# Optimization experiments

Hardware: AMD Instinct MI355X
Metric: run time of the kernel (lower is better)

Reference implementation:

```python
import jax, jax.numpy as jnp
import numpy as np


def setup_inputs() -> dict:
    key = jax.random.key(0)
    B, T, I, H = 64, 512, 1024, 1024
    ks = jax.random.split(key, 9)
    scale_x = 1.0 / np.sqrt(I)
    scale_h = 1.0 / np.sqrt(H)
    inp = {"x": jax.random.normal(ks[0], (B, T, I), jnp.float32)}
    names = [("wxi", "whi"), ("wxf", "whf"), ("wxg", "whg"), ("wxo", "who")]
    for g, (nx, nh) in enumerate(names):
        inp[nx] = jax.random.normal(ks[1 + 2 * g], (I, H), jnp.float32) * scale_x
        inp[nh] = jax.random.normal(ks[2 + 2 * g], (H, H), jnp.float32) * scale_h
    for b in ["bxi", "bhi", "bxf", "bhf", "bxg", "bhg", "bxo", "bho"]:
        inp[b] = jnp.zeros((H,), jnp.float32)
    return inp


def reference(x, wxi, bxi, whi, bhi, wxf, bxf, whf, bhf,
              wxg, bxg, whg, bhg, wxo, bxo, who, bho):
    B, T, I = x.shape
    H = whi.shape[0]
    # Precompute all input projections in one big GEMM: (B,T,4H)
    wx = jnp.concatenate([wxi, wxf, wxg, wxo], axis=1)            # (I,4H)
    bx = jnp.concatenate([bxi + bhi, bxf + bhf, bxg + bhg, bxo + bho])  # fold both biases
    xproj = jnp.einsum('bti,ih->bth', x, wx) + bx                 # (B,T,4H)
    wh = jnp.concatenate([whi, whf, whg, who], axis=1)            # (H,4H)

    def step(carry, xp_t):
        h, c = carry                                              # (B,H) each
        gates = xp_t + h @ wh                                     # (B,4H)
        i, f, g, o = jnp.split(gates, 4, axis=-1)
        i = jax.nn.sigmoid(i)
        f = jax.nn.sigmoid(f)
        g = jnp.tanh(g)
        o = jax.nn.sigmoid(o)
        c = f * c + i * g
        h = o * jnp.tanh(c)
        return (h, c), None

    h0 = jnp.zeros((B, H), x.dtype)
    c0 = jnp.zeros((B, H), x.dtype)
    (h_t, c_t), _ = jax.lax.scan(step, (h0, c0), jnp.swapaxes(xproj, 0, 1))
    return (h_t, c_t)
```

## Files before the change

### kernel.cpp

```cpp
#include <hip/hip_runtime.h>

typedef short bf16x8 __attribute__((ext_vector_type(8)));
typedef float f32x4 __attribute__((ext_vector_type(4)));
typedef unsigned long long u64x2 __attribute__((ext_vector_type(2)));

__device__ __forceinline__ unsigned short f2bf(float f) {
  unsigned u = __float_as_uint(f);
  unsigned r = (u + 0x7FFFu + ((u >> 16) & 1u)) >> 16;
  return (unsigned short)r;
}
__device__ __forceinline__ float bf2f(unsigned short s) {
  return __uint_as_float(((unsigned)s) << 16);
}
__device__ __forceinline__ float sigm(float x) {
  return __builtin_amdgcn_rcpf(1.f + __expf(-x));
}
__device__ __forceinline__ float tanh_a(float x) {
  return 1.f - 2.f * __builtin_amdgcn_rcpf(__expf(2.f * x) + 1.f);
}

__device__ __forceinline__ void gload_lds16(const void* g, void* l) {
  __builtin_amdgcn_global_load_lds(
      (const __attribute__((address_space(1))) unsigned int*)g,
      (__attribute__((address_space(3))) unsigned int*)l, 16, 0, 0);
}

#define ALOAD(p)     __hip_atomic_load((p), __ATOMIC_RELAXED, __HIP_MEMORY_SCOPE_AGENT)
#define ASTORE(p, v) __hip_atomic_store((p), (v), __ATOMIC_RELAXED, __HIP_MEMORY_SCOPE_AGENT)


__global__ void k_cvt_x(const float* __restrict__ x, unsigned short* __restrict__ xb, int n4) {
  int i = blockIdx.x * blockDim.x + threadIdx.x;
  if (i < n4) {
    float4 v = ((const float4*)x)[i];
    ushort4 o;
    o.x = f2bf(v.x); o.y = f2bf(v.y); o.z = f2bf(v.z); o.w = f2bf(v.w);
    ((ushort4*)xb)[i] = o;
  }
}

__global__ void k_pack_w(const float* __restrict__ wxi, const float* __restrict__ wxf,
                         const float* __restrict__ wxg, const float* __restrict__ wxo,
                         const float* __restrict__ whi, const float* __restrict__ whf,
                         const float* __restrict__ whg, const float* __restrict__ who,
                         unsigned short* __restrict__ wxt, unsigned short* __restrict__ whp) {
  const float* srcs[8] = {wxi, wxf, wxg, wxo, whi, whf, whg, who};
  int slab = blockIdx.z;
  const float* src = srcs[slab];
  int gate = slab & 3;
  bool is_wh = slab >= 4;
  __shared__ float tile[32][33];
  int tx = threadIdx.x, ty = threadIdx.y;
  int j0 = blockIdx.x * 32, k0 = blockIdx.y * 32;
  #pragma unroll
  for (int i = 0; i < 32; i += 8)
    tile[ty + i][tx] = src[(size_t)(k0 + ty + i) * 1024 + j0 + tx];
  __syncthreads();
  unsigned short* dst = is_wh ? whp : wxt;
  #pragma unroll
  for (int i = 0; i < 32; i += 8) {
    int j = j0 + ty + i;
    int k = k0 + tx;
    float v = tile[tx][ty + i];
    int row = is_wh ? ((j >> 2) * 16 + gate * 4 + (j & 3)) : (gate * 1024 + j);
    dst[(size_t)row * 1024 + k] = f2bf(v);
  }
}

__global__ void k_bias(const float* bxi, const float* bhi, const float* bxf, const float* bhf,
                       const float* bxg, const float* bhg, const float* bxo, const float* bho,
                       float* __restrict__ bx4) {
  int n = blockIdx.x * 256 + threadIdx.x;
  int gate = n >> 10, j = n & 1023;
  const float* a = gate == 0 ? bxi : gate == 1 ? bxf : gate == 2 ? bxg : bxo;
  const float* b = gate == 0 ? bhi : gate == 1 ? bhf : gate == 2 ? bhg : bho;
  bx4[n] = a[j] + b[j];
}

__global__ void k_init(unsigned short* __restrict__ hbuf, unsigned int* __restrict__ flags) {
  int i = blockIdx.x * 256 + threadIdx.x;
  ASTORE((unsigned long long*)hbuf + i, 0ull);
  if (i < 256) ASTORE(flags + i, 0u);
}


__global__ __launch_bounds__(256) void k_xproj(
    const unsigned short* __restrict__ xb,
    const unsigned short* __restrict__ wxt,
    const float* __restrict__ bx4,
    unsigned short* __restrict__ xp)
{
  __shared__ __align__(16) short As[128 * 64];
  __shared__ __align__(16) short Bs[128 * 64];
  const int tid = threadIdx.x;
  const int bid = blockIdx.x;
  const int m0 = (bid >> 5) * 128;
  const int n0 = (bid & 31) * 128;
  const int lane = tid & 63, w = tid >> 6;
  const int l15 = lane & 15, hi = lane >> 4;
  const int mrow0 = (w >> 1) * 64, ncol0 = (w & 1) * 64;

  f32x4 acc[4][4] = {};
  const char* xbB = (const char*)xb;
  const char* wtB = (const char*)wxt;

  for (int ks = 0; ks < 16; ++ks) {
    #pragma unroll
    for (int c = 0; c < 4; ++c) {
      int d = c * 4096 + tid * 16;
      int r = d >> 7;
      int kb = (d & 127) ^ ((r & 7) << 4);
      gload_lds16(xbB + ((size_t)(m0 + r) * 2048 + ks * 128 + kb), (char*)As + d);
    }
    #pragma unroll
    for (int c = 0; c < 4; ++c) {
      int d = c * 4096 + tid * 16;
      int r = d >> 7;
      int kb = (d & 127) ^ ((r & 7) << 4);
      gload_lds16(wtB + ((size_t)(n0 + r) * 2048 + ks * 128 + kb), (char*)Bs + d);
    }
    __syncthreads();
    #pragma unroll
    for (int kk = 0; kk < 2; ++kk) {
      bf16x8 a[4], b[4];
      #pragma unroll
      for (int mt = 0; mt < 4; ++mt) {
        int r = mrow0 + mt * 16 + l15;
        int byt = r * 128 + ((kk * 64 + hi * 16) ^ ((r & 7) << 4));
        a[mt] = *(const bf16x8*)((const char*)As + byt);
      }
      #pragma unroll
      for (int nt = 0; nt < 4; ++nt) {
        int r = ncol0 + nt * 16 + l15;
        int byt = r * 128 + ((kk * 64 + hi * 16) ^ ((r & 7) << 4));
        b[nt] = *(const bf16x8*)((const char*)Bs + byt);
      }
      #pragma unroll
      for (int mt = 0; mt < 4; ++mt)
        #pragma unroll
        for (int nt = 0; nt < 4; ++nt)
          acc[mt][nt] = __builtin_amdgcn_mfma_f32_16x16x32_bf16(a[mt], b[nt], acc[mt][nt], 0, 0, 0);
    }
    __syncthreads();
  }
  float bias[4];
  int pcol[4];
  #pragma unroll
  for (int nt = 0; nt < 4; ++nt) {
    int n = n0 + ncol0 + nt * 16 + l15;
    bias[nt] = bx4[n];
    int gate = n >> 10, j = n & 1023;
    pcol[nt] = (j >> 2) * 16 + gate * 4 + (j & 3);
  }
  #pragma unroll
  for (int mt = 0; mt < 4; ++mt)
    #pragma unroll
    for (int nt = 0; nt < 4; ++nt) {
      #pragma unroll
      for (int ri = 0; ri < 4; ++ri) {
        int row = m0 + mrow0 + mt * 16 + hi * 4 + ri;
        int prow = (row & 511) * 64 + (row >> 9);
        xp[(size_t)prow * 4096 + pcol[nt]] = f2bf(acc[mt][nt][ri] + bias[nt]);
      }
    }
}


__global__ __launch_bounds__(512, 1) void k_lstm(
    const unsigned short* __restrict__ whp,
    const unsigned short* __restrict__ xp,
    unsigned short* __restrict__ hbuf,
    unsigned int* __restrict__ flags,
    float* __restrict__ out)
{
  const int bid = blockIdx.x;
  const int q = bid >> 5;
  const int cg = bid & 31;
  const int r0 = q * 16;
  const int tid = threadIdx.x;
  const int lane = tid & 63, w = tid >> 6;
  const int l15 = lane & 15, hi = lane >> 4;
  const int gate = l15 >> 2, jj = l15 & 3;

  __shared__ __align__(16) short hs[16 * 1032];

  const unsigned short* wrow = whp + (size_t)((8 * cg + w) * 16 + l15) * 1024 + hi * 8;
  bf16x8 wf[32];
  #pragma unroll
  for (int ks = 0; ks < 32; ++ks) wf[ks] = *(const bf16x8*)(wrow + ks * 32);
  #pragma unroll
  for (int ks = 0; ks < 32; ++ks) asm volatile("" : "+v"(wf[ks]));

  const int hcol = 32 * cg + 4 * w + jj;
  const int pc = (8 * cg + w) * 16 + l15;
  const int base = (lane & 48) | jj;
  const int pbase = lane & 48;
  const int srow = tid >> 5;
  const int scp = tid & 31;
  float cst[4] = {0.f, 0.f, 0.f, 0.f};

  float xpv[4];
  #pragma unroll
  for (int ri = 0; ri < 4; ++ri)
    xpv[ri] = bf2f(xp[(size_t)(r0 + hi * 4 + ri) * 4096 + pc]);

  for (int t = 0; t < 512; ++t) {
    {
      const char* gsrc = (const char*)(hbuf + (t & 1) * 65536 + (r0 + srow) * 1024) + scp * 16;
      u64x2 tmp[4];
      #pragma unroll
      for (int i = 0; i < 4; ++i)
        asm volatile("global_load_dwordx4 %0, %1, off sc0 sc1"
                     : "=v"(tmp[i]) : "v"(gsrc + i * 512) : "memory");
      asm volatile("s_waitcnt vmcnt(0)" ::: "memory");
      __builtin_amdgcn_sched_barrier(0);
      short* ld = hs + srow * 1032 + scp * 8;
      #pragma unroll
      for (int i = 0; i < 4; ++i)
        *(bf16x8*)(ld + i * 256) = __builtin_bit_cast(bf16x8, tmp[i]);
    }
    __syncthreads();

    const short* hsrow = hs + l15 * 1032 + hi * 8;
    f32x4 ac0 = {}, ac1 = {}, ac2 = {}, ac3 = {};
    #pragma unroll
    for (int ks = 0; ks < 32; ks += 4) {
      ac0 = __builtin_amdgcn_mfma_f32_16x16x32_bf16(*(const bf16x8*)(hsrow + ks * 32),       wf[ks],     ac0, 0, 0, 0);
      ac1 = __builtin_amdgcn_mfma_f32_16x16x32_bf16(*(const bf16x8*)(hsrow + (ks + 1) * 32), wf[ks + 1], ac1, 0, 0, 0);
      ac2 = __builtin_amdgcn_mfma_f32_16x16x32_bf16(*(const bf16x8*)(hsrow + (ks + 2) * 32), wf[ks + 2], ac2, 0, 0, 0);
      ac3 = __builtin_amdgcn_mfma_f32_16x16x32_bf16(*(const bf16x8*)(hsrow + (ks + 3) * 32), wf[ks + 3], ac3, 0, 0, 0);
    }
    f32x4 acc = (ac0 + ac1) + (ac2 + ac3);

    float act[4];
    #pragma unroll
    for (int ri = 0; ri < 4; ++ri) {
      float v = acc[ri] + xpv[ri];
      act[ri] = (gate == 2) ? tanh_a(v) : sigm(v);
    }
    float hv[4];
    #pragma unroll
    for (int ri = 0; ri < 4; ++ri) {
      float iv = __shfl(act[ri], base);
      float fv = __shfl(act[ri], base + 4);
      float gv = __shfl(act[ri], base + 8);
      float ov = __shfl(act[ri], base + 12);
      cst[ri] = fv * cst[ri] + iv * gv;
      hv[ri] = ov * tanh_a(cst[ri]);
    }

    if (t == 511) {
      if (gate == 0) {
        #pragma unroll
        for (int ri = 0; ri < 4; ++ri) {
          int b = r0 + hi * 4 + ri;
          out[b * 1024 + hcol] = hv[ri];
          out[65536 + b * 1024 + hcol] = cst[ri];
        }
      }
      break;
    }

    unsigned short* hn = hbuf + ((t + 1) & 1) * 65536;
    #pragma unroll
    for (int ri = 0; ri < 4; ++ri) {
      int hbv = (int)f2bf(hv[ri]);
      int c0 = __shfl(hbv, pbase + 0);
      int c1 = __shfl(hbv, pbase + 1);
      int c2 = __shfl(hbv, pbase + 2);
      int c3 = __shfl(hbv, pbase + 3);
      if (l15 == 0) {
        unsigned lo = ((unsigned)c0 & 0xFFFFu) | ((unsigned)c1 << 16);
        unsigned long long hi64 = ((unsigned)c2 & 0xFFFFu) | ((unsigned)c3 << 16);
        unsigned long long pv = (unsigned long long)lo | (hi64 << 32);
        int row = r0 + hi * 4 + ri;
        ASTORE((unsigned long long*)(hn + row * 1024 + 32 * cg + 4 * w), pv);
      }
    }

    __syncthreads();
    if (tid == 0) ASTORE(flags + bid, (unsigned)(t + 1));

    float nx[4];
    #pragma unroll
    for (int ri = 0; ri < 4; ++ri)
      nx[ri] = bf2f(xp[(size_t)((t + 1) * 64 + r0 + hi * 4 + ri) * 4096 + pc]);

    {
      const unsigned int* fp = flags + q * 32 + (lane & 31);
      unsigned tgt = (unsigned)(t + 1);
      while (true) {
        unsigned f = ALOAD(fp);
        if (__all(f >= tgt)) break;
      }
    }
    #pragma unroll
    for (int ri = 0; ri < 4; ++ri) xpv[ri] = nx[ri];
  }
}


extern "C" void kernel_launch(void* const* d_in, const int* in_sizes, int n_in,
                              void* d_out, int out_size, void* d_ws, size_t ws_size,
                              hipStream_t stream) {
  const float* x = (const float*)d_in[0];
  const float* wxi = (const float*)d_in[1];
  const float* whi = (const float*)d_in[2];
  const float* wxf = (const float*)d_in[3];
  const float* whf = (const float*)d_in[4];
  const float* wxg = (const float*)d_in[5];
  const float* whg = (const float*)d_in[6];
  const float* wxo = (const float*)d_in[7];
  const float* who = (const float*)d_in[8];

  char* ws = (char*)d_ws;
  unsigned short* xb  = (unsigned short*)(ws);
  unsigned short* wxt = (unsigned short*)(ws + 67108864);
  unsigned short* whp = (unsigned short*)(ws + 75497472);
  unsigned short* xpj = (unsigned short*)(ws + 83886080);
  float*          bx4 = (float*)(ws + 352321536);
  unsigned short* hbuf  = (unsigned short*)(ws + 352337920);
  unsigned int*   flags = (unsigned int*)(ws + 352337920 + 262144);

  k_cvt_x<<<32768, 256, 0, stream>>>(x, xb, 8388608);
  k_pack_w<<<dim3(32, 32, 8), dim3(32, 8), 0, stream>>>(wxi, wxf, wxg, wxo, whi, whf, whg, who, wxt, whp);
  k_bias<<<16, 256, 0, stream>>>((const float*)d_in[9], (const float*)d_in[10],
                                 (const float*)d_in[11], (const float*)d_in[12],
                                 (const float*)d_in[13], (const float*)d_in[14],
                                 (const float*)d_in[15], (const float*)d_in[16], bx4);
  k_init<<<128, 256, 0, stream>>>(hbuf, flags);
  k_xproj<<<8192, 256, 0, stream>>>(xb, wxt, bx4, xpj);

  float* out = (float*)d_out;
  void* args[] = {(void*)&whp, (void*)&xpj, (void*)&hbuf, (void*)&flags, (void*)&out};
  hipLaunchCooperativeKernel((const void*)k_lstm, dim3(128), dim3(512), args, 0, stream);
}
```

Before: 2.326 ms.

## Replace per-block barrier flags with per-wave flags polled before h load

Each wave now publishes its own step counter after its h stores drain, instead of a block-wide __syncthreads followed by a single thread writing a per-block flag. Each wave polls all 256 per-wave flags of its batch group with one 16-byte load per lane, and this poll moves to the start of the next step. The aim is to drop a block barrier and let waves start sooner. It also removes the empty asm that pinned the weight registers, which may change register allocation and risks spills or reloads.

```diff
diff --git a/kernel.cpp b/kernel.cpp
--- a/kernel.cpp
+++ b/kernel.cpp
@@ -2,6 +2,7 @@
 
 typedef short bf16x8 __attribute__((ext_vector_type(8)));
 typedef float f32x4 __attribute__((ext_vector_type(4)));
+typedef unsigned int u32x4 __attribute__((ext_vector_type(4)));
 typedef unsigned long long u64x2 __attribute__((ext_vector_type(2)));
 
 __device__ __forceinline__ unsigned short f2bf(float f) {
@@ -77,10 +78,10 @@
   bx4[n] = a[j] + b[j];
 }
 
-__global__ void k_init(unsigned short* __restrict__ hbuf, unsigned int* __restrict__ flags) {
+__global__ void k_init(unsigned short* __restrict__ hbuf, unsigned int* __restrict__ wflags) {
   int i = blockIdx.x * 256 + threadIdx.x;
   ASTORE((unsigned long long*)hbuf + i, 0ull);
-  if (i < 256) ASTORE(flags + i, 0u);
+  if (i < 1024) ASTORE(wflags + i, 0u);
 }
 
 
@@ -170,7 +171,7 @@
     const unsigned short* __restrict__ whp,
     const unsigned short* __restrict__ xp,
     unsigned short* __restrict__ hbuf,
-    unsigned int* __restrict__ flags,
+    unsigned int* __restrict__ wflags,
     float* __restrict__ out)
 {
   const int bid = blockIdx.x;
@@ -188,8 +189,6 @@
   bf16x8 wf[32];
   #pragma unroll
   for (int ks = 0; ks < 32; ++ks) wf[ks] = *(const bf16x8*)(wrow + ks * 32);
-  #pragma unroll
-  for (int ks = 0; ks < 32; ++ks) asm volatile("" : "+v"(wf[ks]));
 
   const int hcol = 32 * cg + 4 * w + jj;
   const int pc = (8 * cg + w) * 16 + l15;
@@ -197,6 +196,8 @@
   const int pbase = lane & 48;
   const int srow = tid >> 5;
   const int scp = tid & 31;
+  const unsigned int* fpoll = wflags + q * 256 + lane * 4;
+  unsigned int* fown = wflags + q * 256 + cg * 8 + w;
   float cst[4] = {0.f, 0.f, 0.f, 0.f};
 
   float xpv[4];
@@ -205,6 +206,19 @@
     xpv[ri] = bf2f(xp[(size_t)(r0 + hi * 4 + ri) * 4096 + pc]);
 
   for (int t = 0; t < 512; ++t) {
+    if (t > 0) {
+      const unsigned tgt = (unsigned)t;
+      while (true) {
+        u32x4 f;
+        asm volatile("global_load_dwordx4 %0, %1, off sc0 sc1"
+                     : "=v"(f) : "v"(fpoll) : "memory");
+        asm volatile("s_waitcnt vmcnt(0)" ::: "memory");
+        __builtin_amdgcn_sched_barrier(0);
+        bool ok = (f.x >= tgt) & (f.y >= tgt) & (f.z >= tgt) & (f.w >= tgt);
+        if (__all(ok)) break;
+      }
+    }
+
     {
       const char* gsrc = (const char*)(hbuf + (t & 1) * 65536 + (r0 + srow) * 1024) + scp * 16;
       u64x2 tmp[4];
@@ -278,22 +292,13 @@
       }
     }
 
-    __syncthreads();
-    if (tid == 0) ASTORE(flags + bid, (unsigned)(t + 1));
+    asm volatile("s_waitcnt vmcnt(0)" ::: "memory");
+    if (lane == 0) ASTORE(fown, (unsigned)(t + 1));
 
     float nx[4];
     #pragma unroll
     for (int ri = 0; ri < 4; ++ri)
       nx[ri] = bf2f(xp[(size_t)((t + 1) * 64 + r0 + hi * 4 + ri) * 4096 + pc]);
-
-    {
-      const unsigned int* fp = flags + q * 32 + (lane & 31);
-      unsigned tgt = (unsigned)(t + 1);
-      while (true) {
-        unsigned f = ALOAD(fp);
-        if (__all(f >= tgt)) break;
-      }
-    }
     #pragma unroll
     for (int ri = 0; ri < 4; ++ri) xpv[ri] = nx[ri];
   }
@@ -319,8 +324,8 @@
   unsigned short* whp = (unsigned short*)(ws + 75497472);
   unsigned short* xpj = (unsigned short*)(ws + 83886080);
   float*          bx4 = (float*)(ws + 352321536);
-  unsigned short* hbuf  = (unsigned short*)(ws + 352337920);
-  unsigned int*   flags = (unsigned int*)(ws + 352337920 + 262144);
+  unsigned short* hbuf   = (unsigned short*)(ws + 352337920);
+  unsigned int*   wflags = (unsigned int*)(ws + 352337920 + 262144);
 
   k_cvt_x<<<32768, 256, 0, stream>>>(x, xb, 8388608);
   k_pack_w<<<dim3(32, 32, 8), dim3(32, 8), 0, stream>>>(wxi, wxf, wxg, wxo, whi, whf, whg, who, wxt, whp);
@@ -328,10 +333,10 @@
                                  (const float*)d_in[11], (const float*)d_in[12],
                                  (const float*)d_in[13], (const float*)d_in[14],
                                  (const float*)d_in[15], (const float*)d_in[16], bx4);
-  k_init<<<128, 256, 0, stream>>>(hbuf, flags);
+  k_init<<<128, 256, 0, stream>>>(hbuf, wflags);
   k_xproj<<<8192, 256, 0, stream>>>(xb, wxt, bx4, xpj);
 
   float* out = (float*)d_out;
-  void* args[] = {(void*)&whp, (void*)&xpj, (void*)&hbuf, (void*)&flags, (void*)&out};
+  void* args[] = {(void*)&whp, (void*)&xpj, (void*)&hbuf, (void*)&wflags, (void*)&out};
   hipLaunchCooperativeKernel((const void*)k_lstm, dim3(128), dim3(512), args, 0, stream);
 }
```

Result: slower. 2.465 ms (+6.0%).

## Fuse input projection into recurrent kernel with producer blocks and per-step flags

Applied to the files above, without the earlier changes.

Removes the separate x-projection GEMM and launches one cooperative kernel of 256 blocks. Blocks 128 and up compute the x-projection one timestep at a time and publish per-step flags, while the first 128 blocks run the LSTM recurrence and spin on those flags before loading each step's projection. The projection output is relaid out so each lane's four batch values come from one 8-byte load. The aim is to hide the GEMM behind the latency-bound recurrence. The cost is smaller, less efficient GEMM tiles that reload x and weights, and the spin-waits that depend on the producer keeping ahead of the consumer.

```diff
diff --git a/kernel.cpp b/kernel.cpp
--- a/kernel.cpp
+++ b/kernel.cpp
@@ -2,6 +2,8 @@
 
 typedef short bf16x8 __attribute__((ext_vector_type(8)));
 typedef float f32x4 __attribute__((ext_vector_type(4)));
+typedef unsigned int u32x2 __attribute__((ext_vector_type(2)));
+typedef unsigned int u32x4 __attribute__((ext_vector_type(4)));
 typedef unsigned long long u64x2 __attribute__((ext_vector_type(2)));
 
 __device__ __forceinline__ unsigned short f2bf(float f) {
@@ -43,7 +45,7 @@
                          const float* __restrict__ wxg, const float* __restrict__ wxo,
                          const float* __restrict__ whi, const float* __restrict__ whf,
                          const float* __restrict__ whg, const float* __restrict__ who,
-                         unsigned short* __restrict__ wxt, unsigned short* __restrict__ whp) {
+                         unsigned short* __restrict__ wxtp, unsigned short* __restrict__ whp) {
   const float* srcs[8] = {wxi, wxf, wxg, wxo, whi, whf, whg, who};
   int slab = blockIdx.z;
   const float* src = srcs[slab];
@@ -56,140 +58,125 @@
   for (int i = 0; i < 32; i += 8)
     tile[ty + i][tx] = src[(size_t)(k0 + ty + i) * 1024 + j0 + tx];
   __syncthreads();
-  unsigned short* dst = is_wh ? whp : wxt;
+  unsigned short* dst = is_wh ? whp : wxtp;
   #pragma unroll
   for (int i = 0; i < 32; i += 8) {
     int j = j0 + ty + i;
     int k = k0 + tx;
     float v = tile[tx][ty + i];
-    int row = is_wh ? ((j >> 2) * 16 + gate * 4 + (j & 3)) : (gate * 1024 + j);
+    int row = (j >> 2) * 16 + gate * 4 + (j & 3);
     dst[(size_t)row * 1024 + k] = f2bf(v);
   }
 }
 
 __global__ void k_bias(const float* bxi, const float* bhi, const float* bxf, const float* bhf,
                        const float* bxg, const float* bhg, const float* bxo, const float* bho,
-                       float* __restrict__ bx4) {
+                       float* __restrict__ pbx4) {
   int n = blockIdx.x * 256 + threadIdx.x;
   int gate = n >> 10, j = n & 1023;
   const float* a = gate == 0 ? bxi : gate == 1 ? bxf : gate == 2 ? bxg : bxo;
   const float* b = gate == 0 ? bhi : gate == 1 ? bhf : gate == 2 ? bhg : bho;
-  bx4[n] = a[j] + b[j];
-}
-
-__global__ void k_init(unsigned short* __restrict__ hbuf, unsigned int* __restrict__ flags) {
+  int pcol = (j >> 2) * 16 + gate * 4 + (j & 3);
+  pbx4[pcol] = a[j] + b[j];
+}
+
+__global__ void k_init(unsigned short* __restrict__ hbuf, unsigned int* __restrict__ flags,
+                       unsigned int* __restrict__ xflags) {
   int i = blockIdx.x * 256 + threadIdx.x;
   ASTORE((unsigned long long*)hbuf + i, 0ull);
-  if (i < 256) ASTORE(flags + i, 0u);
-}
-
-
-__global__ __launch_bounds__(256) void k_xproj(
+  if (i < 128) ASTORE(flags + i, 0u);
+  if (i < 16384) ASTORE(xflags + i, 0u);
+}
+
+
+__global__ __launch_bounds__(512, 1) void k_fused(
     const unsigned short* __restrict__ xb,
-    const unsigned short* __restrict__ wxt,
-    const float* __restrict__ bx4,
-    unsigned short* __restrict__ xp)
+    const unsigned short* __restrict__ wxtp,
+    const unsigned short* __restrict__ whp,
+    const float* __restrict__ pbx4,
+    unsigned short* __restrict__ xp,
+    unsigned short* __restrict__ hbuf,
+    unsigned int* __restrict__ flags,
+    unsigned int* __restrict__ xflags,
+    float* __restrict__ out)
 {
-  __shared__ __align__(16) short As[128 * 64];
-  __shared__ __align__(16) short Bs[128 * 64];
+  __shared__ __align__(16) short smem[16 * 1032];
+  const int bid = blockIdx.x;
   const int tid = threadIdx.x;
-  const int bid = blockIdx.x;
-  const int m0 = (bid >> 5) * 128;
-  const int n0 = (bid & 31) * 128;
   const int lane = tid & 63, w = tid >> 6;
   const int l15 = lane & 15, hi = lane >> 4;
-  const int mrow0 = (w >> 1) * 64, ncol0 = (w & 1) * 64;
-
-  f32x4 acc[4][4] = {};
-  const char* xbB = (const char*)xb;
-  const char* wtB = (const char*)wxt;
-
-  for (int ks = 0; ks < 16; ++ks) {
-    #pragma unroll
-    for (int c = 0; c < 4; ++c) {
-      int d = c * 4096 + tid * 16;
-      int r = d >> 7;
-      int kb = (d & 127) ^ ((r & 7) << 4);
-      gload_lds16(xbB + ((size_t)(m0 + r) * 2048 + ks * 128 + kb), (char*)As + d);
-    }
-    #pragma unroll
-    for (int c = 0; c < 4; ++c) {
-      int d = c * 4096 + tid * 16;
-      int r = d >> 7;
-      int kb = (d & 127) ^ ((r & 7) << 4);
-      gload_lds16(wtB + ((size_t)(n0 + r) * 2048 + ks * 128 + kb), (char*)Bs + d);
-    }
-    __syncthreads();
-    #pragma unroll
-    for (int kk = 0; kk < 2; ++kk) {
-      bf16x8 a[4], b[4];
+
+  if (bid >= 128) {
+    const int wid = bid - 128;
+    const int s = wid >> 2, ph = wid & 3;
+    short* As = smem;
+    short* Bs = smem + 4096;
+    const char* xbB = (const char*)xb;
+    const char* wtB = (const char*)wxtp;
+    const int pcl = w * 16 + l15;
+    const int pcg = 128 * s + pcl;
+    const float bias = pbx4[pcg];
+
+    for (int t = ph; t < 512; t += 4) {
+      f32x4 acc[4] = {};
+      for (int ks = 0; ks < 16; ++ks) {
+        {
+          int d = tid * 16;
+          int r = d >> 7;
+          int kb = (d & 127) ^ ((r & 7) << 4);
+          gload_lds16(xbB + ((size_t)(r * 512 + t) * 2048 + ks * 128 + kb), (char*)As + d);
+        }
+        #pragma unroll
+        for (int c = 0; c < 2; ++c) {
+          int d = c * 8192 + tid * 16;
+          int r = d >> 7;
+          int kb = (d & 127) ^ ((r & 7) << 4);
+          gload_lds16(wtB + ((size_t)(128 * s + r) * 2048 + ks * 128 + kb), (char*)Bs + d);
+        }
+        __syncthreads();
+        #pragma unroll
+        for (int kk = 0; kk < 2; ++kk) {
+          bf16x8 bfr;
+          {
+            int r = pcl;
+            int byt = r * 128 + ((kk * 64 + hi * 16) ^ ((r & 7) << 4));
+            bfr = *(const bf16x8*)((const char*)Bs + byt);
+          }
+          #pragma unroll
+          for (int mt = 0; mt < 4; ++mt) {
+            int r = mt * 16 + l15;
+            int byt = r * 128 + ((kk * 64 + hi * 16) ^ ((r & 7) << 4));
+            bf16x8 afr = *(const bf16x8*)((const char*)As + byt);
+            acc[mt] = __builtin_amdgcn_mfma_f32_16x16x32_bf16(afr, bfr, acc[mt], 0, 0, 0);
+          }
+        }
+        __syncthreads();
+      }
       #pragma unroll
       for (int mt = 0; mt < 4; ++mt) {
-        int r = mrow0 + mt * 16 + l15;
-        int byt = r * 128 + ((kk * 64 + hi * 16) ^ ((r & 7) << 4));
-        a[mt] = *(const bf16x8*)((const char*)As + byt);
-      }
-      #pragma unroll
-      for (int nt = 0; nt < 4; ++nt) {
-        int r = ncol0 + nt * 16 + l15;
-        int byt = r * 128 + ((kk * 64 + hi * 16) ^ ((r & 7) << 4));
-        b[nt] = *(const bf16x8*)((const char*)Bs + byt);
-      }
-      #pragma unroll
-      for (int mt = 0; mt < 4; ++mt)
-        #pragma unroll
-        for (int nt = 0; nt < 4; ++nt)
-          acc[mt][nt] = __builtin_amdgcn_mfma_f32_16x16x32_bf16(a[mt], b[nt], acc[mt][nt], 0, 0, 0);
-    }
-    __syncthreads();
+        unsigned h0 = f2bf(acc[mt][0] + bias), h1 = f2bf(acc[mt][1] + bias);
+        unsigned h2 = f2bf(acc[mt][2] + bias), h3 = f2bf(acc[mt][3] + bias);
+        unsigned long long pv = (unsigned long long)(h0 | (h1 << 16)) |
+                                ((unsigned long long)(h2 | (h3 << 16)) << 32);
+        size_t ei = ((size_t)t * 4096 + pcg) * 16 + mt * 4 + hi;
+        ASTORE((unsigned long long*)xp + ei, pv);
+      }
+      __syncthreads();
+      if (tid == 0) ASTORE(xflags + t * 32 + s, 1u);
+    }
+    return;
   }
-  float bias[4];
-  int pcol[4];
-  #pragma unroll
-  for (int nt = 0; nt < 4; ++nt) {
-    int n = n0 + ncol0 + nt * 16 + l15;
-    bias[nt] = bx4[n];
-    int gate = n >> 10, j = n & 1023;
-    pcol[nt] = (j >> 2) * 16 + gate * 4 + (j & 3);
-  }
-  #pragma unroll
-  for (int mt = 0; mt < 4; ++mt)
-    #pragma unroll
-    for (int nt = 0; nt < 4; ++nt) {
-      #pragma unroll
-      for (int ri = 0; ri < 4; ++ri) {
-        int row = m0 + mrow0 + mt * 16 + hi * 4 + ri;
-        int prow = (row & 511) * 64 + (row >> 9);
-        xp[(size_t)prow * 4096 + pcol[nt]] = f2bf(acc[mt][nt][ri] + bias[nt]);
-      }
-    }
-}
-
-
-__global__ __launch_bounds__(512, 1) void k_lstm(
-    const unsigned short* __restrict__ whp,
-    const unsigned short* __restrict__ xp,
-    unsigned short* __restrict__ hbuf,
-    unsigned int* __restrict__ flags,
-    float* __restrict__ out)
-{
-  const int bid = blockIdx.x;
+
   const int q = bid >> 5;
   const int cg = bid & 31;
   const int r0 = q * 16;
-  const int tid = threadIdx.x;
-  const int lane = tid & 63, w = tid >> 6;
-  const int l15 = lane & 15, hi = lane >> 4;
   const int gate = l15 >> 2, jj = l15 & 3;
-
-  __shared__ __align__(16) short hs[16 * 1032];
+  short* hs = smem;
 
   const unsigned short* wrow = whp + (size_t)((8 * cg + w) * 16 + l15) * 1024 + hi * 8;
   bf16x8 wf[32];
   #pragma unroll
   for (int ks = 0; ks < 32; ++ks) wf[ks] = *(const bf16x8*)(wrow + ks * 32);
-  #pragma unroll
-  for (int ks = 0; ks < 32; ++ks) asm volatile("" : "+v"(wf[ks]));
 
   const int hcol = 32 * cg + 4 * w + jj;
   const int pc = (8 * cg + w) * 16 + l15;
@@ -199,10 +186,17 @@
   const int scp = tid & 31;
   float cst[4] = {0.f, 0.f, 0.f, 0.f};
 
+  while (ALOAD(xflags + cg) == 0) {}
+  u32x2 nf;
+  asm volatile("global_load_dwordx2 %0, %1, off sc0 sc1"
+               : "=v"(nf) : "v"((const char*)xp + ((size_t)pc * 64 + r0 + hi * 4) * 2) : "memory");
+  asm volatile("s_waitcnt vmcnt(0)" ::: "memory");
+  __builtin_amdgcn_sched_barrier(0);
   float xpv[4];
-  #pragma unroll
-  for (int ri = 0; ri < 4; ++ri)
-    xpv[ri] = bf2f(xp[(size_t)(r0 + hi * 4 + ri) * 4096 + pc]);
+  xpv[0] = bf2f((unsigned short)(nf.x & 0xFFFFu));
+  xpv[1] = bf2f((unsigned short)(nf.x >> 16));
+  xpv[2] = bf2f((unsigned short)(nf.y & 0xFFFFu));
+  xpv[3] = bf2f((unsigned short)(nf.y >> 16));
 
   for (int t = 0; t < 512; ++t) {
     {
@@ -281,10 +275,11 @@
     __syncthreads();
     if (tid == 0) ASTORE(flags + bid, (unsigned)(t + 1));
 
-    float nx[4];
-    #pragma unroll
-    for (int ri = 0; ri < 4; ++ri)
-      nx[ri] = bf2f(xp[(size_t)((t + 1) * 64 + r0 + hi * 4 + ri) * 4096 + pc]);
+    while (ALOAD(xflags + (t + 1) * 32 + cg) == 0) {}
+    asm volatile("global_load_dwordx2 %0, %1, off sc0 sc1"
+                 : "=v"(nf)
+                 : "v"((const char*)xp + (((size_t)(t + 1) * 4096 + pc) * 64 + r0 + hi * 4) * 2)
+                 : "memory");
 
     {
       const unsigned int* fp = flags + q * 32 + (lane & 31);
@@ -294,8 +289,12 @@
         if (__all(f >= tgt)) break;
       }
     }
-    #pragma unroll
-    for (int ri = 0; ri < 4; ++ri) xpv[ri] = nx[ri];
+    asm volatile("s_waitcnt vmcnt(0)" ::: "memory");
+    __builtin_amdgcn_sched_barrier(0);
+    xpv[0] = bf2f((unsigned short)(nf.x & 0xFFFFu));
+    xpv[1] = bf2f((unsigned short)(nf.x >> 16));
+    xpv[2] = bf2f((unsigned short)(nf.y & 0xFFFFu));
+    xpv[3] = bf2f((unsigned short)(nf.y >> 16));
   }
 }
 
@@ -314,24 +313,25 @@
   const float* who = (const float*)d_in[8];
 
   char* ws = (char*)d_ws;
-  unsigned short* xb  = (unsigned short*)(ws);
-  unsigned short* wxt = (unsigned short*)(ws + 67108864);
-  unsigned short* whp = (unsigned short*)(ws + 75497472);
-  unsigned short* xpj = (unsigned short*)(ws + 83886080);
-  float*          bx4 = (float*)(ws + 352321536);
+  unsigned short* xb    = (unsigned short*)(ws);
+  unsigned short* wxtp  = (unsigned short*)(ws + 67108864);
+  unsigned short* whp   = (unsigned short*)(ws + 75497472);
+  unsigned short* xpj   = (unsigned short*)(ws + 83886080);
+  float*          pbx4  = (float*)(ws + 352321536);
   unsigned short* hbuf  = (unsigned short*)(ws + 352337920);
-  unsigned int*   flags = (unsigned int*)(ws + 352337920 + 262144);
+  unsigned int*   flags = (unsigned int*)(ws + 352600064);
+  unsigned int*   xflags= (unsigned int*)(ws + 352604160);
 
   k_cvt_x<<<32768, 256, 0, stream>>>(x, xb, 8388608);
-  k_pack_w<<<dim3(32, 32, 8), dim3(32, 8), 0, stream>>>(wxi, wxf, wxg, wxo, whi, whf, whg, who, wxt, whp);
+  k_pack_w<<<dim3(32, 32, 8), dim3(32, 8), 0, stream>>>(wxi, wxf, wxg, wxo, whi, whf, whg, who, wxtp, whp);
   k_bias<<<16, 256, 0, stream>>>((const float*)d_in[9], (const float*)d_in[10],
                                  (const float*)d_in[11], (const float*)d_in[12],
                                  (const float*)d_in[13], (const float*)d_in[14],
-                                 (const float*)d_in[15], (const float*)d_in[16], bx4);
-  k_init<<<128, 256, 0, stream>>>(hbuf, flags);
-  k_xproj<<<8192, 256, 0, stream>>>(xb, wxt, bx4, xpj);
+                                 (const float*)d_in[15], (const float*)d_in[16], pbx4);
+  k_init<<<128, 256, 0, stream>>>(hbuf, flags, xflags);
 
   float* out = (float*)d_out;
-  void* args[] = {(void*)&whp, (void*)&xpj, (void*)&hbuf, (void*)&flags, (void*)&out};
-  hipLaunchCooperativeKernel((const void*)k_lstm, dim3(128), dim3(512), args, 0, stream);
-}
+  void* args[] = {(void*)&xb, (void*)&wxtp, (void*)&whp, (void*)&pbx4,
+                  (void*)&xpj, (void*)&hbuf, (void*)&flags, (void*)&xflags, (void*)&out};
+  hipLaunchCooperativeKernel((const void*)k_fused, dim3(256), dim3(512), args, 0, stream);
+}
```

After: 2.457 ms. 5.6% more time.
